# Kernel tuning notes

Measured on AMD Instinct MI355X. Metric: run time of the kernel, lower is better.

The kernel has to match this reference:

```python
import jax, jax.numpy as jnp
import numpy as np

DIM = 768
N_IMGS = 1024
N_PATCH = 196
GRID = int(np.sqrt(N_PATCH))  # 14
B = 64


def setup_inputs() -> dict:
    key = jax.random.key(0)
    ks = jax.random.split(key, 12)
    x = jax.random.normal(ks[0], (B, N_PATCH, DIM), dtype=jnp.float32)
    mask = jnp.ones((B, N_PATCH), dtype=jnp.bool_)
    img_ids = jax.random.randint(ks[1], (B,), 0, N_IMGS, dtype=jnp.int32)
    eps = jax.random.normal(ks[2], (B, 2, N_PATCH), dtype=jnp.float32)
    s = 0.02
    Wq = jax.random.normal(ks[3], (DIM, DIM), dtype=jnp.float32) * s
    bq = jnp.zeros((DIM,), dtype=jnp.float32)
    Wk = jax.random.normal(ks[4], (DIM, DIM), dtype=jnp.float32) * s
    bk = jnp.zeros((DIM,), dtype=jnp.float32)
    Wv = jax.random.normal(ks[5], (DIM, DIM), dtype=jnp.float32) * s
    bv = jnp.zeros((DIM,), dtype=jnp.float32)
    # per-image Gaussian location params: means in [0, GRID-1], small positive stds
    avgs = jax.random.uniform(ks[6], (N_IMGS, 2, N_PATCH), dtype=jnp.float32) * (GRID - 1)
    std_devs = jax.random.uniform(ks[7], (N_IMGS, 2, N_PATCH), dtype=jnp.float32) * 1.5 + 0.1
    return {"x": x, "mask": mask, "img_ids": img_ids, "eps": eps,
            "Wq": Wq, "bq": bq, "Wk": Wk, "bk": bk, "Wv": Wv, "bv": bv,
            "avgs": avgs, "std_devs": std_devs}


def reference(x, mask, img_ids, eps, Wq, bq, Wk, bk, Wv, bv, avgs, std_devs):
    # projections: (B,S,D)
    q = jnp.einsum('bsd,ed->bse', x, Wq) + bq
    k = jnp.einsum('bsd,ed->bse', x, Wk) + bk
    v = jnp.einsum('bsd,ed->bse', x, Wv) + bv

    # sample per-query key coordinates: torch.normal(mean, std) == mean + std * eps
    mu = avgs[img_ids]        # (B,2,S)
    sd = std_devs[img_ids]    # (B,2,S)
    coord = mu + sd * eps     # (B,2,S)
    kx, ky = coord[:, 0], coord[:, 1]           # each (B,S)
    kx1, kx2 = jnp.ceil(kx), jnp.floor(kx)
    ky1, ky2 = jnp.ceil(ky), jnp.floor(ky)

    # 4 interpolation-corner flat indices per query: grid*y + x  -> (B,S,4)
    idx = jnp.stack([GRID * ky1 + kx1,
                     GRID * ky1 + kx2,
                     GRID * ky2 + kx1,
                     GRID * ky2 + kx2], axis=-1)
    idx = jnp.clip(idx, 0, N_PATCH - 1).astype(jnp.int32)

    bidx = jnp.arange(idx.shape[0])[:, None, None]  # (B,1,1)
    sampled_k = k[bidx, idx]  # (B,S,4,D)
    sampled_v = v[bidx, idx]  # (B,S,4,D)

    # softmax over the 4 sampled keys (elementwise per feature), weighted sum of values
    w = jax.nn.softmax(q[:, :, None, :] * sampled_k, axis=2)  # (B,S,4,D)
    out = jnp.sum(w * sampled_v, axis=2)                      # (B,S,D)
    return out
```

## Files before the change

kernel.cpp:

```cpp
#include <hip/hip_runtime.h>
#include <hip/hip_bf16.h>

typedef _Float16 f16;
typedef f16 f16x4 __attribute__((ext_vector_type(4)));
typedef f16 f16x8 __attribute__((ext_vector_type(8)));
typedef float f32x4 __attribute__((ext_vector_type(4)));

#define DIM   768
#define NP    196
#define BATCH 64
#define MROWS (BATCH * NP)
#define NCOLS (3 * DIM)
#define GRIDF 14.0f

#define NW4   (DIM * DIM / 4)
#define NB4   (NCOLS / 4)
#define NWCVT (3 * NW4 + NB4)

__global__ __launch_bounds__(256) void convert_w(
    const float* __restrict__ Wq, const float* __restrict__ Wk, const float* __restrict__ Wv,
    const float* __restrict__ bq, const float* __restrict__ bk, const float* __restrict__ bv,
    f16* __restrict__ W_h, float* __restrict__ bias_all) {
  int i = blockIdx.x * 256 + threadIdx.x;
  if (i >= NWCVT) return;
  if (i < 3 * NW4) {
    const float* src;
    f16* dst;
    int j = i;
    if (j < NW4)          { src = Wq; dst = W_h; }
    else if (j < 2 * NW4) { src = Wk; dst = W_h + DIM * DIM;     j -= NW4; }
    else                  { src = Wv; dst = W_h + 2 * DIM * DIM; j -= 2 * NW4; }
    float4 v = ((const float4*)src)[j];
    f16x4 h;
    h[0] = (f16)v.x; h[1] = (f16)v.y; h[2] = (f16)v.z; h[3] = (f16)v.w;
    ((f16x4*)dst)[j] = h;
  } else {
    int j = i - 3 * NW4;
    float4 v = (j < 192) ? ((const float4*)bq)[j]
             : (j < 384) ? ((const float4*)bk)[j - 192]
                         : ((const float4*)bv)[j - 384];
    ((float4*)bias_all)[j] = v;
  }
}


#define BM 256
#define BN 256
#define BK 64
#define NT    (DIM / BK)
#define NITER (NT / 2)

__device__ __forceinline__ void gl_lds16(const f16* g, f16* l) {
  __builtin_amdgcn_global_load_lds(
      (const __attribute__((address_space(1))) void*)g,
      (__attribute__((address_space(3))) void*)l, 16, 0, 0);
}

#define MFMA16(acc_, av, bv) acc_ = __builtin_amdgcn_mfma_f32_16x16x32_f16(av, bv, acc_, 0, 0, 0)
#define BAR    __builtin_amdgcn_s_barrier()
#define LGKM0  asm volatile("s_waitcnt lgkmcnt(0)" ::: "memory")
#define VMCNT4 asm volatile("s_waitcnt vmcnt(4)" ::: "memory")
#define VMCNT0 asm volatile("s_waitcnt vmcnt(0)" ::: "memory")

#define sAoff(buf) ((buf) * (BM * BK))
#define sBoff(buf) (2 * BM * BK + (buf) * (BN * BK))

__global__ __launch_bounds__(512, 2) void gemm_qkv(
    const float* __restrict__ X, const f16* __restrict__ W,
    const float* __restrict__ bias_all, f16* __restrict__ C) {
  __shared__ __align__(16) f16 lds[2 * BM * BK + 2 * BN * BK];

  const int t    = threadIdx.x;
  const int lane = t & 63;
  const int wid  = t >> 6;
  const int wr   = wid >> 2;
  const int wc   = wid & 3;

  const int nwg = 49 * 9, qq = nwg / 8, rr = nwg % 8;
  const int xcd = blockIdx.x & 7, seq = blockIdx.x >> 3;
  const int logical = (xcd < rr ? xcd * (qq + 1) : rr * (qq + 1) + (xcd - rr) * qq) + seq;
  const int bm0 = (logical / 9) * BM;
  const int bn0 = (logical % 9) * BN;

  const int srow  = t >> 3;
  const int sslot = t & 7;
  const int gcol  = 8 * (sslot ^ (srow & 7));
  const int lds_off = srow * BK + sslot * 8;
  const f16* gBr = W + (size_t)(bn0 + srow) * DIM + gcol;

  float4 pA0, pA1, pA2, pA3, pA4, pA5, pA6, pA7;

#define A_ISSUE(kt) do {                                                      \
    const float* _g0 = X + (size_t)(bm0 + srow) * DIM + (kt) * BK + gcol;     \
    pA0 = *(const float4*)_g0;               pA1 = *(const float4*)(_g0 + 4); \
    pA2 = *(const float4*)(_g0 + 64 * DIM);  pA3 = *(const float4*)(_g0 + 64 * DIM + 4);  \
    pA4 = *(const float4*)(_g0 + 128 * DIM); pA5 = *(const float4*)(_g0 + 128 * DIM + 4); \
    pA6 = *(const float4*)(_g0 + 192 * DIM); pA7 = *(const float4*)(_g0 + 192 * DIM + 4); \
  } while (0)

#define CVT8(dst_, lo_, hi_) do {                                  \
    dst_[0]=(f16)lo_.x; dst_[1]=(f16)lo_.y; dst_[2]=(f16)lo_.z; dst_[3]=(f16)lo_.w; \
    dst_[4]=(f16)hi_.x; dst_[5]=(f16)hi_.y; dst_[6]=(f16)hi_.z; dst_[7]=(f16)hi_.w; } while (0)

#define A_WRITE(kt, h) do {                                                   \
    f16x8 _h0, _h1;                                                           \
    if ((h) == 0) { CVT8(_h0, pA0, pA1); CVT8(_h1, pA2, pA3); }               \
    else          { CVT8(_h0, pA4, pA5); CVT8(_h1, pA6, pA7); }               \
    f16* _l = &lds[sAoff((kt) & 1) + (h) * 128 * BK + lds_off];               \
    *(f16x8*)_l = _h0; *(f16x8*)(_l + 64 * BK) = _h1;                         \
  } while (0)

#define STAGE_B(kt, h) do {                                                   \
    const f16* _g = gBr + (size_t)((h) * 128) * DIM + (kt) * BK;              \
    f16* _l = &lds[sBoff((kt) & 1) + (h) * 128 * BK + lds_off];               \
    gl_lds16(_g, _l);                                                         \
    gl_lds16(_g + (size_t)64 * DIM, _l + 64 * BK);                            \
  } while (0)

  const int rl = lane & 15;
  const int kg = lane >> 4;
  const int s7 = lane & 7;
  const int slot0 = ((0 * 4 + kg) ^ s7) * 8;
  const int slot1 = ((1 * 4 + kg) ^ s7) * 8;
  const int aBase = (wr * 128 + rl) * BK;
  const int bBase = (wc * 64 + rl) * BK;

  f32x4 acc[8][4] = {};
  f16x8 afr[2][2], bfr[4][2];

#define LDB(buf) do {                                                                   \
    _Pragma("unroll") for (int ni = 0; ni < 4; ++ni) {                                  \
      bfr[ni][0] = *(const f16x8*)&lds[sBoff(buf) + bBase + ni * 16 * BK + slot0];      \
      bfr[ni][1] = *(const f16x8*)&lds[sBoff(buf) + bBase + ni * 16 * BK + slot1];      \
    } } while (0)

#define LDA(buf, q_) do {                                                               \
    _Pragma("unroll") for (int mm = 0; mm < 2; ++mm) {                                  \
      afr[mm][0] = *(const f16x8*)&lds[sAoff(buf) + aBase + ((q_) * 2 + mm) * 16 * BK + slot0]; \
      afr[mm][1] = *(const f16x8*)&lds[sAoff(buf) + aBase + ((q_) * 2 + mm) * 16 * BK + slot1]; \
    } } while (0)

#define MMA(q_) do {                                                                    \
    __builtin_amdgcn_s_setprio(1);                                                      \
    _Pragma("unroll") for (int ni = 0; ni < 4; ++ni) {                                  \
      MFMA16(acc[(q_) * 2 + 0][ni], bfr[ni][0], afr[0][0]);                             \
      MFMA16(acc[(q_) * 2 + 1][ni], bfr[ni][0], afr[1][0]);                             \
      MFMA16(acc[(q_) * 2 + 0][ni], bfr[ni][1], afr[0][1]);                             \
      MFMA16(acc[(q_) * 2 + 1][ni], bfr[ni][1], afr[1][1]);                             \
    }                                                                                   \
    __builtin_amdgcn_s_setprio(0); } while (0)

  A_ISSUE(0);
  STAGE_B(0, 0); STAGE_B(0, 1);
  STAGE_B(1, 0); STAGE_B(1, 1);
  A_WRITE(0, 0); A_WRITE(0, 1);
  VMCNT4;
  LGKM0;
  BAR;

  for (int i = 0; i < NITER; ++i) {
    const int t1 = 2 * i + 1;
    const bool more = (i + 1 < NITER);
    A_ISSUE(t1);
    LDB(0); LDA(0, 0);
    A_WRITE(t1, 0);
    BAR; LGKM0; MMA(0); BAR;
    LDA(0, 1); A_WRITE(t1, 1);
    BAR; LGKM0; MMA(1); BAR;
    LDA(0, 2); if (more) STAGE_B(t1 + 1, 0);
    BAR; LGKM0; MMA(2); BAR;
    LDA(0, 3); if (more) STAGE_B(t1 + 1, 1);
    BAR; LGKM0; MMA(3);
    if (more) { VMCNT4; } else { VMCNT0; }
    BAR;
    if (more) A_ISSUE(t1 + 1);
    LDB(1); LDA(1, 0);
    if (more) A_WRITE(t1 + 1, 0);
    BAR; LGKM0; MMA(0); BAR;
    LDA(1, 1); if (more) A_WRITE(t1 + 1, 1);
    BAR; LGKM0; MMA(1); BAR;
    LDA(1, 2); if (more) STAGE_B(t1 + 2, 0);
    BAR; LGKM0; MMA(2); BAR;
    LDA(1, 3); if (more) STAGE_B(t1 + 2, 1);
    BAR; LGKM0; MMA(3); VMCNT4; BAR;
  }

  {
    const int mloc0 = wr * 128 + rl;
    const int nq0   = wc * 64 + 4 * kg;
#pragma unroll
    for (int ni = 0; ni < 4; ++ni) {
      const int nloc = nq0 + ni * 16;
      const float4 b4 = *(const float4*)&bias_all[bn0 + nloc];
#pragma unroll
      for (int mi = 0; mi < 8; ++mi) {
        const int m = mloc0 + mi * 16;
        f16x4 h;
        h[0] = (f16)(acc[mi][ni][0] + b4.x);
        h[1] = (f16)(acc[mi][ni][1] + b4.y);
        h[2] = (f16)(acc[mi][ni][2] + b4.z);
        h[3] = (f16)(acc[mi][ni][3] + b4.w);
        *(f16x4*)&lds[m * 256 + (nloc ^ ((m & 7) << 3))] = h;
      }
    }
    LGKM0; BAR;
    const int rrow = t >> 5;
    const int rchk = t & 31;
#pragma unroll
    for (int p = 0; p < 16; ++p) {
      const int row = p * 16 + rrow;
      f16x8 vdat = *(const f16x8*)&lds[row * 256 + ((rchk * 8) ^ ((row & 7) << 3))];
      *(f16x8*)&C[(size_t)(bm0 + row) * NCOLS + bn0 + rchk * 8] = vdat;
    }
  }
}

__global__ __launch_bounds__(256) void attend(
    const f16* __restrict__ qkv,
    const int* __restrict__ img_ids, const float* __restrict__ eps,
    const float* __restrict__ avgs, const float* __restrict__ stds,
    float* __restrict__ out) {
  const int lane = threadIdx.x & 63;
  const int wid  = threadIdx.x >> 6;
  const int logical = (blockIdx.x & 7) * 392 + (blockIdx.x >> 3);
  const int gw = logical * 4 + wid;
  const int b = gw / NP;
  const int s = gw - b * NP;

  const int img = img_ids[b];
  const float ex = eps[(b * 2 + 0) * NP + s];
  const float ey = eps[(b * 2 + 1) * NP + s];
  const float mux = avgs[(img * 2 + 0) * NP + s];
  const float muy = avgs[(img * 2 + 1) * NP + s];
  const float sdx = stds[(img * 2 + 0) * NP + s];
  const float sdy = stds[(img * 2 + 1) * NP + s];

  const float kx = fmaf(sdx, ex, mux);
  const float ky = fmaf(sdy, ey, muy);
  const float kx1 = ceilf(kx), kx2 = floorf(kx);
  const float ky1 = ceilf(ky), ky2 = floorf(ky);

  int idx[4];
  idx[0] = (int)fminf(fmaxf(GRIDF * ky1 + kx1, 0.0f), 195.0f);
  idx[1] = (int)fminf(fmaxf(GRIDF * ky1 + kx2, 0.0f), 195.0f);
  idx[2] = (int)fminf(fmaxf(GRIDF * ky2 + kx1, 0.0f), 195.0f);
  idx[3] = (int)fminf(fmaxf(GRIDF * ky2 + kx2, 0.0f), 195.0f);

  const f16* qrow = qkv + (size_t)gw * NCOLS;
  const f16* base = qkv + (size_t)(b * NP) * NCOLS;
  const f16* k0p = base + (size_t)idx[0] * NCOLS + DIM;
  const f16* k1p = base + (size_t)idx[1] * NCOLS + DIM;
  const f16* k2p = base + (size_t)idx[2] * NCOLS + DIM;
  const f16* k3p = base + (size_t)idx[3] * NCOLS + DIM;
  const f16* v0p = k0p + DIM;
  const f16* v1p = k1p + DIM;
  const f16* v2p = k2p + DIM;
  const f16* v3p = k3p + DIM;
  float* orow = out + (size_t)gw * DIM;

#pragma unroll
  for (int seg = 0; seg < 3; ++seg) {
    const int e0 = seg * 256 + lane * 4;
    f16x4 qv  = *(const f16x4*)(qrow + e0);
    f16x4 kv0 = *(const f16x4*)(k0p + e0);
    f16x4 kv1 = *(const f16x4*)(k1p + e0);
    f16x4 kv2 = *(const f16x4*)(k2p + e0);
    f16x4 kv3 = *(const f16x4*)(k3p + e0);
    f16x4 vv0 = *(const f16x4*)(v0p + e0);
    f16x4 vv1 = *(const f16x4*)(v1p + e0);
    f16x4 vv2 = *(const f16x4*)(v2p + e0);
    f16x4 vv3 = *(const f16x4*)(v3p + e0);
    float4 o;
    float* op = &o.x;
#pragma unroll
    for (int c = 0; c < 4; ++c) {
      const float q = (float)qv[c];
      const float s0 = q * (float)kv0[c];
      const float s1 = q * (float)kv1[c];
      const float s2 = q * (float)kv2[c];
      const float s3 = q * (float)kv3[c];
      const float mx = fmaxf(fmaxf(s0, s1), fmaxf(s2, s3));
      const float w0 = __expf(s0 - mx);
      const float w1 = __expf(s1 - mx);
      const float w2 = __expf(s2 - mx);
      const float w3 = __expf(s3 - mx);
      const float den = w0 + w1 + w2 + w3;
      const float num = w0 * (float)vv0[c] + w1 * (float)vv1[c] +
                        w2 * (float)vv2[c] + w3 * (float)vv3[c];
      op[c] = num / den;
    }
    *(float4*)(orow + e0) = o;
  }
}

extern "C" void kernel_launch(void* const* d_in, const int* in_sizes, int n_in,
                              void* d_out, int out_size, void* d_ws, size_t ws_size,
                              hipStream_t stream) {
  const float* x       = (const float*)d_in[0];
  const int*   img_ids = (const int*)d_in[2];
  const float* eps     = (const float*)d_in[3];
  const float* Wq      = (const float*)d_in[4];
  const float* bq      = (const float*)d_in[5];
  const float* Wk      = (const float*)d_in[6];
  const float* bk      = (const float*)d_in[7];
  const float* Wv      = (const float*)d_in[8];
  const float* bv      = (const float*)d_in[9];
  const float* avgs    = (const float*)d_in[10];
  const float* stds    = (const float*)d_in[11];
  float* out = (float*)d_out;

  char* ws = (char*)d_ws;
  const size_t WH_BYTES = (size_t)NCOLS * DIM * 2;
  const size_t BI_BYTES = (size_t)NCOLS * 4;
  f16*   W_h      = (f16*)ws;
  float* bias_all = (float*)(ws + WH_BYTES);
  f16*   qkv      = (f16*)(ws + WH_BYTES + BI_BYTES);

  {
    int grid = (NWCVT + 255) / 256;
    convert_w<<<grid, 256, 0, stream>>>(Wq, Wk, Wv, bq, bk, bv, W_h, bias_all);
  }
  {
    gemm_qkv<<<441, 512, 0, stream>>>(x, W_h, bias_all, qkv);
  }
  {
    int grid = MROWS / 4;
    attend<<<grid, 256, 0, stream>>>(qkv, img_ids, eps, avgs, stds, out);
  }
}
```

Before: 96.21 us.

## Pre-convert activations to fp16 and stage A tiles via direct global-to-LDS loads

Adds a pass to the conversion kernel that casts x to fp16 into a workspace buffer. The GEMM then stages A tiles with the same direct global-to-LDS loads used for B, dropping the register-held fp32 loads, in-loop conversion and explicit LDS stores. This removes register pressure and VALU work from the GEMM main loop and lets A loads run asynchronously. The cost is an extra full read and write of x in a separate launch, which may outweigh the GEMM savings.

```diff
diff --git a/kernel.cpp b/kernel.cpp
--- a/kernel.cpp
+++ b/kernel.cpp
@@ -13,29 +13,35 @@
 #define NCOLS (3 * DIM)
 #define GRIDF 14.0f
 
+#define NX4   (MROWS * DIM / 4)
 #define NW4   (DIM * DIM / 4)
 #define NB4   (NCOLS / 4)
-#define NWCVT (3 * NW4 + NB4)
-
-__global__ __launch_bounds__(256) void convert_w(
+#define NCVTA (NX4 + 3 * NW4 + NB4)
+
+__global__ __launch_bounds__(256) void convert_inputs(
+    const float* __restrict__ x,
     const float* __restrict__ Wq, const float* __restrict__ Wk, const float* __restrict__ Wv,
     const float* __restrict__ bq, const float* __restrict__ bk, const float* __restrict__ bv,
-    f16* __restrict__ W_h, float* __restrict__ bias_all) {
+    f16* __restrict__ x_h, f16* __restrict__ W_h, float* __restrict__ bias_all) {
   int i = blockIdx.x * 256 + threadIdx.x;
-  if (i >= NWCVT) return;
-  if (i < 3 * NW4) {
+  if (i >= NCVTA) return;
+  if (i < NX4 + 3 * NW4) {
     const float* src;
     f16* dst;
-    int j = i;
-    if (j < NW4)          { src = Wq; dst = W_h; }
-    else if (j < 2 * NW4) { src = Wk; dst = W_h + DIM * DIM;     j -= NW4; }
-    else                  { src = Wv; dst = W_h + 2 * DIM * DIM; j -= 2 * NW4; }
+    int j;
+    if (i < NX4) { src = x; dst = x_h; j = i; }
+    else {
+      j = i - NX4;
+      if (j < NW4)          { src = Wq; dst = W_h; }
+      else if (j < 2 * NW4) { src = Wk; dst = W_h + DIM * DIM;     j -= NW4; }
+      else                  { src = Wv; dst = W_h + 2 * DIM * DIM; j -= 2 * NW4; }
+    }
     float4 v = ((const float4*)src)[j];
     f16x4 h;
     h[0] = (f16)v.x; h[1] = (f16)v.y; h[2] = (f16)v.z; h[3] = (f16)v.w;
     ((f16x4*)dst)[j] = h;
   } else {
-    int j = i - 3 * NW4;
+    int j = i - (NX4 + 3 * NW4);
     float4 v = (j < 192) ? ((const float4*)bq)[j]
              : (j < 384) ? ((const float4*)bk)[j - 192]
                          : ((const float4*)bv)[j - 384];
@@ -66,7 +72,7 @@
 #define sBoff(buf) (2 * BM * BK + (buf) * (BN * BK))
 
 __global__ __launch_bounds__(512, 2) void gemm_qkv(
-    const float* __restrict__ X, const f16* __restrict__ W,
+    const f16* __restrict__ A, const f16* __restrict__ W,
     const float* __restrict__ bias_all, f16* __restrict__ C) {
   __shared__ __align__(16) f16 lds[2 * BM * BK + 2 * BN * BK];
 
@@ -86,35 +92,21 @@
   const int sslot = t & 7;
   const int gcol  = 8 * (sslot ^ (srow & 7));
   const int lds_off = srow * BK + sslot * 8;
+  const f16* gAr = A + (size_t)(bm0 + srow) * DIM + gcol;
   const f16* gBr = W + (size_t)(bn0 + srow) * DIM + gcol;
 
-  float4 pA0, pA1, pA2, pA3, pA4, pA5, pA6, pA7;
-
-#define A_ISSUE(kt) do {                                                      \
-    const float* _g0 = X + (size_t)(bm0 + srow) * DIM + (kt) * BK + gcol;     \
-    pA0 = *(const float4*)_g0;               pA1 = *(const float4*)(_g0 + 4); \
-    pA2 = *(const float4*)(_g0 + 64 * DIM);  pA3 = *(const float4*)(_g0 + 64 * DIM + 4);  \
-    pA4 = *(const float4*)(_g0 + 128 * DIM); pA5 = *(const float4*)(_g0 + 128 * DIM + 4); \
-    pA6 = *(const float4*)(_g0 + 192 * DIM); pA7 = *(const float4*)(_g0 + 192 * DIM + 4); \
+#define STAGE_A(kt, h) do {                                          \
+    const f16* _g = gAr + (size_t)((h) * 128) * DIM + (kt) * BK;     \
+    f16* _l = &lds[sAoff((kt) & 1) + (h) * 128 * BK + lds_off];      \
+    gl_lds16(_g, _l);                                                \
+    gl_lds16(_g + (size_t)64 * DIM, _l + 64 * BK);                   \
   } while (0)
 
-#define CVT8(dst_, lo_, hi_) do {                                  \
-    dst_[0]=(f16)lo_.x; dst_[1]=(f16)lo_.y; dst_[2]=(f16)lo_.z; dst_[3]=(f16)lo_.w; \
-    dst_[4]=(f16)hi_.x; dst_[5]=(f16)hi_.y; dst_[6]=(f16)hi_.z; dst_[7]=(f16)hi_.w; } while (0)
-
-#define A_WRITE(kt, h) do {                                                   \
-    f16x8 _h0, _h1;                                                           \
-    if ((h) == 0) { CVT8(_h0, pA0, pA1); CVT8(_h1, pA2, pA3); }               \
-    else          { CVT8(_h0, pA4, pA5); CVT8(_h1, pA6, pA7); }               \
-    f16* _l = &lds[sAoff((kt) & 1) + (h) * 128 * BK + lds_off];               \
-    *(f16x8*)_l = _h0; *(f16x8*)(_l + 64 * BK) = _h1;                         \
-  } while (0)
-
-#define STAGE_B(kt, h) do {                                                   \
-    const f16* _g = gBr + (size_t)((h) * 128) * DIM + (kt) * BK;              \
-    f16* _l = &lds[sBoff((kt) & 1) + (h) * 128 * BK + lds_off];               \
-    gl_lds16(_g, _l);                                                         \
-    gl_lds16(_g + (size_t)64 * DIM, _l + 64 * BK);                            \
+#define STAGE_B(kt, h) do {                                          \
+    const f16* _g = gBr + (size_t)((h) * 128) * DIM + (kt) * BK;     \
+    f16* _l = &lds[sBoff((kt) & 1) + (h) * 128 * BK + lds_off];      \
+    gl_lds16(_g, _l);                                                \
+    gl_lds16(_g + (size_t)64 * DIM, _l + 64 * BK);                   \
   } while (0)
 
   const int rl = lane & 15;
@@ -150,22 +142,17 @@
     }                                                                                   \
     __builtin_amdgcn_s_setprio(0); } while (0)
 
-  A_ISSUE(0);
-  STAGE_B(0, 0); STAGE_B(0, 1);
+  STAGE_A(0, 0); STAGE_A(0, 1); STAGE_B(0, 0); STAGE_B(0, 1);
   STAGE_B(1, 0); STAGE_B(1, 1);
-  A_WRITE(0, 0); A_WRITE(0, 1);
   VMCNT4;
-  LGKM0;
   BAR;
 
   for (int i = 0; i < NITER; ++i) {
     const int t1 = 2 * i + 1;
     const bool more = (i + 1 < NITER);
-    A_ISSUE(t1);
-    LDB(0); LDA(0, 0);
-    A_WRITE(t1, 0);
+    LDB(0); LDA(0, 0); STAGE_A(t1, 0);
     BAR; LGKM0; MMA(0); BAR;
-    LDA(0, 1); A_WRITE(t1, 1);
+    LDA(0, 1); STAGE_A(t1, 1);
     BAR; LGKM0; MMA(1); BAR;
     LDA(0, 2); if (more) STAGE_B(t1 + 1, 0);
     BAR; LGKM0; MMA(2); BAR;
@@ -173,11 +160,9 @@
     BAR; LGKM0; MMA(3);
     if (more) { VMCNT4; } else { VMCNT0; }
     BAR;
-    if (more) A_ISSUE(t1 + 1);
-    LDB(1); LDA(1, 0);
-    if (more) A_WRITE(t1 + 1, 0);
+    LDB(1); LDA(1, 0); if (more) STAGE_A(t1 + 1, 0);
     BAR; LGKM0; MMA(0); BAR;
-    LDA(1, 1); if (more) A_WRITE(t1 + 1, 1);
+    LDA(1, 1); if (more) STAGE_A(t1 + 1, 1);
     BAR; LGKM0; MMA(1); BAR;
     LDA(1, 2); if (more) STAGE_B(t1 + 2, 0);
     BAR; LGKM0; MMA(2); BAR;
@@ -310,18 +295,20 @@
   float* out = (float*)d_out;
 
   char* ws = (char*)d_ws;
+  const size_t XH_BYTES = (size_t)MROWS * DIM * 2;
   const size_t WH_BYTES = (size_t)NCOLS * DIM * 2;
   const size_t BI_BYTES = (size_t)NCOLS * 4;
-  f16*   W_h      = (f16*)ws;
-  float* bias_all = (float*)(ws + WH_BYTES);
-  f16*   qkv      = (f16*)(ws + WH_BYTES + BI_BYTES);
+  f16*   x_h      = (f16*)ws;
+  f16*   W_h      = (f16*)(ws + XH_BYTES);
+  float* bias_all = (float*)(ws + XH_BYTES + WH_BYTES);
+  f16*   qkv      = (f16*)(ws + XH_BYTES + WH_BYTES + BI_BYTES);
 
   {
-    int grid = (NWCVT + 255) / 256;
-    convert_w<<<grid, 256, 0, stream>>>(Wq, Wk, Wv, bq, bk, bv, W_h, bias_all);
+    int grid = (NCVTA + 255) / 256;
+    convert_inputs<<<grid, 256, 0, stream>>>(x, Wq, Wk, Wv, bq, bk, bv, x_h, W_h, bias_all);
   }
   {
-    gemm_qkv<<<441, 512, 0, stream>>>(x, W_h, bias_all, qkv);
+    gemm_qkv<<<441, 512, 0, stream>>>(x_h, W_h, bias_all, qkv);
   }
   {
     int grid = MROWS / 4;
```

New measurement: 83.82 us (median of 2 runs). -12.9%, faster.

## Stage fp32 X directly into LDS via async loads and convert in registers

Applied to the files above, without the earlier changes.

The QKV GEMM now loads the fp32 activation tile straight into LDS with global_load_lds, replacing the register-staged load, convert and LDS-write path. The f16 conversion moves to after the LDS read, just before the MFMAs. BK is halved to 32 to fit the fp32 tile, and the main loop becomes a simpler double-buffered pipeline with split lo/hi MMA halves and partial lgkm waits. The epilogue writes in two 128-row passes to fit the smaller LDS region. The cost is twice as many LDS bytes for A, redundant per-wave conversions, and more k-iterations with barriers.

```diff
diff --git a/kernel.cpp b/kernel.cpp
--- a/kernel.cpp
+++ b/kernel.cpp
@@ -43,14 +43,12 @@
   }
 }
 
-
 #define BM 256
 #define BN 256
-#define BK 64
-#define NT    (DIM / BK)
-#define NITER (NT / 2)
-
-__device__ __forceinline__ void gl_lds16(const f16* g, f16* l) {
+#define BK 32
+#define NT (DIM / BK)
+
+__device__ __forceinline__ void gl_lds16(const void* g, void* l) {
   __builtin_amdgcn_global_load_lds(
       (const __attribute__((address_space(1))) void*)g,
       (__attribute__((address_space(3))) void*)l, 16, 0, 0);
@@ -58,17 +56,15 @@
 
 #define MFMA16(acc_, av, bv) acc_ = __builtin_amdgcn_mfma_f32_16x16x32_f16(av, bv, acc_, 0, 0, 0)
 #define BAR    __builtin_amdgcn_s_barrier()
+#define LGKM8  asm volatile("s_waitcnt lgkmcnt(8)" ::: "memory")
 #define LGKM0  asm volatile("s_waitcnt lgkmcnt(0)" ::: "memory")
-#define VMCNT4 asm volatile("s_waitcnt vmcnt(4)" ::: "memory")
+#define VMCNT6 asm volatile("s_waitcnt vmcnt(6)" ::: "memory")
 #define VMCNT0 asm volatile("s_waitcnt vmcnt(0)" ::: "memory")
-
-#define sAoff(buf) ((buf) * (BM * BK))
-#define sBoff(buf) (2 * BM * BK + (buf) * (BN * BK))
 
 __global__ __launch_bounds__(512, 2) void gemm_qkv(
     const float* __restrict__ X, const f16* __restrict__ W,
     const float* __restrict__ bias_all, f16* __restrict__ C) {
-  __shared__ __align__(16) f16 lds[2 * BM * BK + 2 * BN * BK];
+  __shared__ __align__(16) char lds[98304];
 
   const int t    = threadIdx.x;
   const int lane = t & 63;
@@ -82,135 +78,135 @@
   const int bm0 = (logical / 9) * BM;
   const int bn0 = (logical % 9) * BN;
 
-  const int srow  = t >> 3;
-  const int sslot = t & 7;
-  const int gcol  = 8 * (sslot ^ (srow & 7));
-  const int lds_off = srow * BK + sslot * 8;
-  const f16* gBr = W + (size_t)(bn0 + srow) * DIM + gcol;
-
-  float4 pA0, pA1, pA2, pA3, pA4, pA5, pA6, pA7;
-
-#define A_ISSUE(kt) do {                                                      \
-    const float* _g0 = X + (size_t)(bm0 + srow) * DIM + (kt) * BK + gcol;     \
-    pA0 = *(const float4*)_g0;               pA1 = *(const float4*)(_g0 + 4); \
-    pA2 = *(const float4*)(_g0 + 64 * DIM);  pA3 = *(const float4*)(_g0 + 64 * DIM + 4);  \
-    pA4 = *(const float4*)(_g0 + 128 * DIM); pA5 = *(const float4*)(_g0 + 128 * DIM + 4); \
-    pA6 = *(const float4*)(_g0 + 192 * DIM); pA7 = *(const float4*)(_g0 + 192 * DIM + 4); \
-  } while (0)
-
-#define CVT8(dst_, lo_, hi_) do {                                  \
-    dst_[0]=(f16)lo_.x; dst_[1]=(f16)lo_.y; dst_[2]=(f16)lo_.z; dst_[3]=(f16)lo_.w; \
-    dst_[4]=(f16)hi_.x; dst_[5]=(f16)hi_.y; dst_[6]=(f16)hi_.z; dst_[7]=(f16)hi_.w; } while (0)
-
-#define A_WRITE(kt, h) do {                                                   \
-    f16x8 _h0, _h1;                                                           \
-    if ((h) == 0) { CVT8(_h0, pA0, pA1); CVT8(_h1, pA2, pA3); }               \
-    else          { CVT8(_h0, pA4, pA5); CVT8(_h1, pA6, pA7); }               \
-    f16* _l = &lds[sAoff((kt) & 1) + (h) * 128 * BK + lds_off];               \
-    *(f16x8*)_l = _h0; *(f16x8*)(_l + 64 * BK) = _h1;                         \
-  } while (0)
-
-#define STAGE_B(kt, h) do {                                                   \
-    const f16* _g = gBr + (size_t)((h) * 128) * DIM + (kt) * BK;              \
-    f16* _l = &lds[sBoff((kt) & 1) + (h) * 128 * BK + lds_off];               \
-    gl_lds16(_g, _l);                                                         \
-    gl_lds16(_g + (size_t)64 * DIM, _l + 64 * BK);                            \
+  const int srA = t >> 3;
+  const int ssA = t & 7;
+  const int gcA = 4 * (ssA ^ (srA & 7));
+  const float* gA = X + (size_t)(bm0 + srA) * DIM + gcA;
+  const int srB = t >> 2;
+  const int ssB = t & 3;
+  const int gcB = 8 * (ssB ^ ((srB >> 1) & 3));
+  const f16* gBp = W + (size_t)(bn0 + srB) * DIM + gcB;
+
+#define STAGE(kt) do {                                                 \
+    const int _b = (kt) & 1;                                           \
+    const float* _ga = gA + (kt) * BK;                                 \
+    char* _la = lds + _b * 32768 + t * 16;                             \
+    gl_lds16(_ga,                     _la);                            \
+    gl_lds16(_ga + (size_t) 64 * DIM, _la + 8192);                     \
+    gl_lds16(_ga + (size_t)128 * DIM, _la + 16384);                    \
+    gl_lds16(_ga + (size_t)192 * DIM, _la + 24576);                    \
+    const f16* _gb = gBp + (kt) * BK;                                  \
+    char* _lb = lds + 65536 + _b * 16384 + t * 16;                     \
+    gl_lds16(_gb,                     _lb);                            \
+    gl_lds16(_gb + (size_t)128 * DIM, _lb + 8192);                     \
   } while (0)
 
   const int rl = lane & 15;
   const int kg = lane >> 4;
-  const int s7 = lane & 7;
-  const int slot0 = ((0 * 4 + kg) ^ s7) * 8;
-  const int slot1 = ((1 * 4 + kg) ^ s7) * 8;
-  const int aBase = (wr * 128 + rl) * BK;
-  const int bBase = (wc * 64 + rl) * BK;
+  const int sA0 = ((2 * kg)     ^ (rl & 7)) * 4;
+  const int sA1 = ((2 * kg + 1) ^ (rl & 7)) * 4;
+  const int sB8 = (kg ^ ((rl >> 1) & 3)) * 8;
+  const int aBase = (wr * 128 + rl) * 32;
+  const int bBase = (wc * 64 + rl) * 32;
 
   f32x4 acc[8][4] = {};
-  f16x8 afr[2][2], bfr[4][2];
-
-#define LDB(buf) do {                                                                   \
-    _Pragma("unroll") for (int ni = 0; ni < 4; ++ni) {                                  \
-      bfr[ni][0] = *(const f16x8*)&lds[sBoff(buf) + bBase + ni * 16 * BK + slot0];      \
-      bfr[ni][1] = *(const f16x8*)&lds[sBoff(buf) + bBase + ni * 16 * BK + slot1];      \
+  f16x8 afrL[4], afrH[4], bfr[4];
+  f32x4 rlo[4][2], rhi[4][2];
+
+#define SAp(b_) ((const float*)(lds + (b_) * 32768))
+#define SBp(b_) ((const f16*)(lds + 65536 + (b_) * 16384))
+
+#define LDB(b_) do {                                                            \
+    _Pragma("unroll") for (int ni = 0; ni < 4; ++ni)                            \
+      bfr[ni] = *(const f16x8*)&SBp(b_)[bBase + ni * 512 + sB8];                \
+    } while (0)
+
+#define LDA_LO(b_) do {                                                         \
+    _Pragma("unroll") for (int mi = 0; mi < 4; ++mi) {                          \
+      rlo[mi][0] = *(const f32x4*)&SAp(b_)[aBase + mi * 512 + sA0];             \
+      rlo[mi][1] = *(const f32x4*)&SAp(b_)[aBase + mi * 512 + sA1];             \
     } } while (0)
 
-#define LDA(buf, q_) do {                                                               \
-    _Pragma("unroll") for (int mm = 0; mm < 2; ++mm) {                                  \
-      afr[mm][0] = *(const f16x8*)&lds[sAoff(buf) + aBase + ((q_) * 2 + mm) * 16 * BK + slot0]; \
-      afr[mm][1] = *(const f16x8*)&lds[sAoff(buf) + aBase + ((q_) * 2 + mm) * 16 * BK + slot1]; \
+#define LDA_HI(b_) do {                                                         \
+    _Pragma("unroll") for (int mi = 0; mi < 4; ++mi) {                          \
+      rhi[mi][0] = *(const f32x4*)&SAp(b_)[aBase + (mi + 4) * 512 + sA0];       \
+      rhi[mi][1] = *(const f32x4*)&SAp(b_)[aBase + (mi + 4) * 512 + sA1];       \
     } } while (0)
 
-#define MMA(q_) do {                                                                    \
-    __builtin_amdgcn_s_setprio(1);                                                      \
-    _Pragma("unroll") for (int ni = 0; ni < 4; ++ni) {                                  \
-      MFMA16(acc[(q_) * 2 + 0][ni], bfr[ni][0], afr[0][0]);                             \
-      MFMA16(acc[(q_) * 2 + 1][ni], bfr[ni][0], afr[1][0]);                             \
-      MFMA16(acc[(q_) * 2 + 0][ni], bfr[ni][1], afr[0][1]);                             \
-      MFMA16(acc[(q_) * 2 + 1][ni], bfr[ni][1], afr[1][1]);                             \
-    }                                                                                   \
+#define CVT8v(dst_, lo_, hi_) do {                                              \
+    dst_[0]=(f16)lo_[0]; dst_[1]=(f16)lo_[1]; dst_[2]=(f16)lo_[2]; dst_[3]=(f16)lo_[3]; \
+    dst_[4]=(f16)hi_[0]; dst_[5]=(f16)hi_[1]; dst_[6]=(f16)hi_[2]; dst_[7]=(f16)hi_[3]; } while (0)
+
+#define CVT_LO do { _Pragma("unroll") for (int mi = 0; mi < 4; ++mi) CVT8v(afrL[mi], rlo[mi][0], rlo[mi][1]); } while (0)
+#define CVT_HI do { _Pragma("unroll") for (int mi = 0; mi < 4; ++mi) CVT8v(afrH[mi], rhi[mi][0], rhi[mi][1]); } while (0)
+
+#define MMA_LO do {                                                              \
+    __builtin_amdgcn_s_setprio(1);                                               \
+    _Pragma("unroll") for (int ni = 0; ni < 4; ++ni)                             \
+      _Pragma("unroll") for (int mi = 0; mi < 4; ++mi)                           \
+        MFMA16(acc[mi][ni], bfr[ni], afrL[mi]);                                  \
     __builtin_amdgcn_s_setprio(0); } while (0)
 
-  A_ISSUE(0);
-  STAGE_B(0, 0); STAGE_B(0, 1);
-  STAGE_B(1, 0); STAGE_B(1, 1);
-  A_WRITE(0, 0); A_WRITE(0, 1);
-  VMCNT4;
-  LGKM0;
+#define MMA_HI do {                                                              \
+    __builtin_amdgcn_s_setprio(1);                                               \
+    _Pragma("unroll") for (int ni = 0; ni < 4; ++ni)                             \
+      _Pragma("unroll") for (int mi = 0; mi < 4; ++mi)                           \
+        MFMA16(acc[mi + 4][ni], bfr[ni], afrH[mi]);                              \
+    __builtin_amdgcn_s_setprio(0); } while (0)
+
+  STAGE(0);
+  STAGE(1);
+  VMCNT6;
   BAR;
 
-  for (int i = 0; i < NITER; ++i) {
-    const int t1 = 2 * i + 1;
-    const bool more = (i + 1 < NITER);
-    A_ISSUE(t1);
-    LDB(0); LDA(0, 0);
-    A_WRITE(t1, 0);
-    BAR; LGKM0; MMA(0); BAR;
-    LDA(0, 1); A_WRITE(t1, 1);
-    BAR; LGKM0; MMA(1); BAR;
-    LDA(0, 2); if (more) STAGE_B(t1 + 1, 0);
-    BAR; LGKM0; MMA(2); BAR;
-    LDA(0, 3); if (more) STAGE_B(t1 + 1, 1);
-    BAR; LGKM0; MMA(3);
-    if (more) { VMCNT4; } else { VMCNT0; }
+  for (int kt = 0; kt < NT; ++kt) {
+    const int b = kt & 1;
+    const bool more = (kt + 2 < NT);
+    LDB(b); LDA_LO(b); LDA_HI(b);
+    LGKM8;
+    CVT_LO;
+    MMA_LO;
+    LGKM0;
+    CVT_HI;
     BAR;
-    if (more) A_ISSUE(t1 + 1);
-    LDB(1); LDA(1, 0);
-    if (more) A_WRITE(t1 + 1, 0);
-    BAR; LGKM0; MMA(0); BAR;
-    LDA(1, 1); if (more) A_WRITE(t1 + 1, 1);
-    BAR; LGKM0; MMA(1); BAR;
-    LDA(1, 2); if (more) STAGE_B(t1 + 2, 0);
-    BAR; LGKM0; MMA(2); BAR;
-    LDA(1, 3); if (more) STAGE_B(t1 + 2, 1);
-    BAR; LGKM0; MMA(3); VMCNT4; BAR;
+    if (more) STAGE(kt + 2);
+    MMA_HI;
+    if (more) { VMCNT6; } else { VMCNT0; }
+    BAR;
   }
 
   {
-    const int mloc0 = wr * 128 + rl;
-    const int nq0   = wc * 64 + 4 * kg;
-#pragma unroll
-    for (int ni = 0; ni < 4; ++ni) {
-      const int nloc = nq0 + ni * 16;
-      const float4 b4 = *(const float4*)&bias_all[bn0 + nloc];
-#pragma unroll
-      for (int mi = 0; mi < 8; ++mi) {
-        const int m = mloc0 + mi * 16;
-        f16x4 h;
-        h[0] = (f16)(acc[mi][ni][0] + b4.x);
-        h[1] = (f16)(acc[mi][ni][1] + b4.y);
-        h[2] = (f16)(acc[mi][ni][2] + b4.z);
-        h[3] = (f16)(acc[mi][ni][3] + b4.w);
-        *(f16x4*)&lds[m * 256 + (nloc ^ ((m & 7) << 3))] = h;
-      }
-    }
-    LGKM0; BAR;
+    f16* eL = (f16*)lds;
+    const int nq0  = wc * 64 + 4 * kg;
     const int rrow = t >> 5;
     const int rchk = t & 31;
 #pragma unroll
-    for (int p = 0; p < 16; ++p) {
-      const int row = p * 16 + rrow;
-      f16x8 vdat = *(const f16x8*)&lds[row * 256 + ((rchk * 8) ^ ((row & 7) << 3))];
-      *(f16x8*)&C[(size_t)(bm0 + row) * NCOLS + bn0 + rchk * 8] = vdat;
+    for (int p = 0; p < 2; ++p) {
+      if (wr == p) {
+#pragma unroll
+        for (int ni = 0; ni < 4; ++ni) {
+          const int nloc = nq0 + ni * 16;
+          const float4 b4 = *(const float4*)&bias_all[bn0 + nloc];
+#pragma unroll
+          for (int mi = 0; mi < 8; ++mi) {
+            const int e = mi * 16 + rl;
+            f16x4 h;
+            h[0] = (f16)(acc[mi][ni][0] + b4.x);
+            h[1] = (f16)(acc[mi][ni][1] + b4.y);
+            h[2] = (f16)(acc[mi][ni][2] + b4.z);
+            h[3] = (f16)(acc[mi][ni][3] + b4.w);
+            *(f16x4*)&eL[e * 256 + (nloc ^ ((e & 7) << 3))] = h;
+          }
+        }
+      }
+      LGKM0; BAR;
+#pragma unroll
+      for (int it = 0; it < 8; ++it) {
+        const int row = it * 16 + rrow;
+        f16x8 vdat = *(const f16x8*)&eL[row * 256 + ((rchk * 8) ^ ((row & 7) << 3))];
+        *(f16x8*)&C[(size_t)(bm0 + p * 128 + row) * NCOLS + bn0 + rchk * 8] = vdat;
+      }
+      LGKM0; BAR;
     }
   }
 }
```

Measured after the change: 103.4 us. 7.5% more time.
